# Kernel tuning notes

Hardware: AMD Instinct MI355X
Metric: run time of the kernel (lower is better)

The kernel has to match this reference:

```python
import jax, jax.numpy as jnp
import numpy as np

PATCH_SIZE = 24
ALPHA = 0.2  # LeakyReLU negative slope


def setup_inputs() -> dict:
    key = jax.random.key(0)
    k_x, k_adj, k_w, k_wc = jax.random.split(key, 4)
    B, T, N, Cin, Cout = 2, 96, 64, 16, 32
    x = jax.random.normal(k_x, (B, T, N, Cin), dtype=jnp.float32)
    adj = jax.random.uniform(k_adj, (N, N), dtype=jnp.float32)  # weighted adjacency in [0,1)
    # xavier_uniform with gain=1.414 on (Cin, Cout)
    limit = 1.414 * float(np.sqrt(6.0 / (Cin + Cout)))
    W = jax.random.uniform(k_w, (Cin, Cout), dtype=jnp.float32, minval=-limit, maxval=limit)
    W_c = jax.random.uniform(k_wc, (Cout,), dtype=jnp.float32, minval=-0.1, maxval=0.1)
    return {"x": x, "adj": adj, "W": W, "W_c": W_c}


def reference(x, adj, W, W_c):
    B, T, N, Cin = x.shape
    P = PATCH_SIZE
    NP = T // P
    Cout = W.shape[1]
    # torch.view semantics == row-major jnp.reshape (faithful, even though it mixes axes)
    x_patched = x.reshape(B, NP, N, P, Cin)
    h = x_patched @ W  # (B, NP, N, P, Cout)
    # vectorized over patches: per-patch outer product over nodes
    e = jnp.einsum('bsipc,bsjpc->bsijpc', h, h)  # (B, NP, N, N, P, Cout)
    e = jnp.where(e >= 0, e, ALPHA * e)  # LeakyReLU
    e = e * adj[None, None, :, :, None, None]
    e = jax.nn.softmax(e, axis=-1)  # softmax over channel dim (as in original)
    # torch.stack(list, dim=4) of (b,i,j,p,c) over patch index -> (B,N,N,P,NP,C)
    e = jnp.transpose(e, (0, 2, 3, 4, 1, 5))
    attention = e.reshape(B, N, N, T, Cout)  # (B, N, N, T, Cout)
    # h_patched.permute(0,2,1,3,4).reshape(B,N,T,C)
    h_flat = jnp.transpose(h, (0, 2, 1, 3, 4)).reshape(B, N, T, Cout)
    # einsum('bnqtc,bntc->bntc') == sum over q then elementwise multiply
    h_prime = attention.sum(axis=2) * h_flat
    return attention, jax.nn.elu(h_prime)
```

## Files before the change

kernel.cpp:

```cpp
#include <hip/hip_runtime.h>
#include <math.h>

#define Bq 2
#define Tq 96
#define Nq 64
#define CIN 16
#define COUT 32
#define PATCH 24
#define NPq 4
#define JC 4
#define JPER (Nq / JC)
#define ATT_SIZE (Bq * Nq * Nq * Tq * COUT)
#define HP_SIZE (Bq * Nq * Tq * COUT)
#define H_ROWS (Bq * NPq * Nq * PATCH)

__global__ __launch_bounds__(256) void h_gemm_kernel(
    const float* __restrict__ x, const float* __restrict__ W,
    float* __restrict__ h) {
    __shared__ float Wl[CIN * COUT];
    __shared__ float xs[8 * CIN];
    int tid = threadIdx.x;
    Wl[tid]       = W[tid];
    Wl[tid + 256] = W[tid + 256];
    if (tid < 8 * CIN) xs[tid] = x[blockIdx.x * (8 * CIN) + tid];
    __syncthreads();
    int rl = tid >> 5;
    int c  = tid & 31;
    float acc = 0.f;
#pragma unroll
    for (int k = 0; k < CIN; ++k)
        acc += xs[rl * CIN + k] * Wl[k * COUT + c];
    h[blockIdx.x * 256 + tid] = acc;
}

__global__ __launch_bounds__(384) void att_kernel(
    const float* __restrict__ h, const float* __restrict__ adj,
    float* __restrict__ att, float* __restrict__ part) {
    const int bi  = blockIdx.x;
    const int jc  = bi >> 9;
    const int r   = bi & 511;
    const int i   = r & 63;
    const int s   = (r >> 6) & 3;
    const int b   = r >> 8;
    const int j0  = jc * JPER;
    const int tid = threadIdx.x;
    const int p   = tid >> 4;
    const int c0  = (tid & 15) * 2;

    __shared__ float adjrow[JPER];
    if (tid < JPER) adjrow[tid] = adj[i * Nq + j0 + tid];
    __syncthreads();

    const float* hb = h + (size_t)((b * NPq + s) * Nq) * (PATCH * COUT);
    const float2 hi = *(const float2*)(hb + (i * PATCH + p) * COUT + c0);

    float acc0 = 0.f, acc1 = 0.f;
    size_t outbase = ((size_t)((b * Nq + i) * Nq + j0) * Tq + (p * NPq + s)) * COUT + c0;
    const size_t jstride = (size_t)Tq * COUT;

#pragma unroll 4
    for (int jj = 0; jj < JPER; ++jj) {
        const float2 hj = *(const float2*)(hb + ((j0 + jj) * PATCH + p) * COUT + c0);
        const float aj = adjrow[jj];

        float e0 = hi.x * hj.x;
        float e1 = hi.y * hj.y;
        e0 = fmaxf(e0, 0.2f * e0) * aj;
        e1 = fmaxf(e1, 0.2f * e1) * aj;

        float ex0 = __expf(e0);
        float ex1 = __expf(e1);
        float sm = ex0 + ex1;
#pragma unroll
        for (int d = 1; d < 16; d <<= 1) sm += __shfl_xor(sm, d);
        const float inv = __builtin_amdgcn_rcpf(sm);
        const float a0 = ex0 * inv;
        const float a1 = ex1 * inv;
        acc0 += a0;
        acc1 += a1;
        *(float2*)(att + outbase + (size_t)jj * jstride) = make_float2(a0, a1);
    }

    const int t = p * NPq + s;
    float* pp = part + (size_t)jc * HP_SIZE
                     + ((size_t)((b * Nq + i) * Tq + t)) * COUT + c0;
    *(float2*)pp = make_float2(acc0, acc1);
}

__global__ __launch_bounds__(256) void hprime_kernel(
    const float* __restrict__ part, const float* __restrict__ h,
    float* __restrict__ hprime) {
    const int vid  = blockIdx.x * 256 + threadIdx.x;
    const int base = vid * 4;
    const int c  = base & 31;
    const int t  = (base >> 5) % Tq;
    const int bi = base / (COUT * Tq);
    const int i  = bi & 63;
    const int b  = bi >> 6;

    float4 a0 = *(const float4*)(part + base);
    float4 a1 = *(const float4*)(part + base + HP_SIZE);
    float4 a2 = *(const float4*)(part + base + 2 * HP_SIZE);
    float4 a3 = *(const float4*)(part + base + 3 * HP_SIZE);

    const int s2 = t / PATCH;
    const int p2 = t % PATCH;
    const float4 hv = *(const float4*)(h + (size_t)((b * NPq + s2) * Nq + i) * (PATCH * COUT)
                                         + p2 * COUT + c);
    float v0 = (a0.x + a1.x + a2.x + a3.x) * hv.x;
    float v1 = (a0.y + a1.y + a2.y + a3.y) * hv.y;
    float v2 = (a0.z + a1.z + a2.z + a3.z) * hv.z;
    float v3 = (a0.w + a1.w + a2.w + a3.w) * hv.w;
    v0 = v0 >= 0.f ? v0 : expm1f(v0);
    v1 = v1 >= 0.f ? v1 : expm1f(v1);
    v2 = v2 >= 0.f ? v2 : expm1f(v2);
    v3 = v3 >= 0.f ? v3 : expm1f(v3);
    *(float4*)(hprime + base) = make_float4(v0, v1, v2, v3);
}

extern "C" void kernel_launch(void* const* d_in, const int* in_sizes, int n_in,
                              void* d_out, int out_size, void* d_ws, size_t ws_size,
                              hipStream_t stream) {
    (void)in_sizes; (void)n_in; (void)out_size; (void)ws_size;
    const float* x   = (const float*)d_in[0];
    const float* adj = (const float*)d_in[1];
    const float* W   = (const float*)d_in[2];

    float* h    = (float*)d_ws;
    float* part = (float*)d_ws + H_ROWS * COUT;
    float* att  = (float*)d_out;
    float* hp   = (float*)d_out + ATT_SIZE;

    hipLaunchKernelGGL(h_gemm_kernel, dim3(H_ROWS / 8), dim3(256), 0, stream,
                       x, W, h);
    hipLaunchKernelGGL(att_kernel, dim3(JC * Bq * NPq * Nq), dim3(384), 0, stream,
                       h, adj, att, part);
    hipLaunchKernelGGL(hprime_kernel, dim3(HP_SIZE / 4 / 256), dim3(256), 0, stream,
                       part, h, hp);
}
```

Measured before the change: 34.66 us.

## Fold patch index into block and widen attention stores to float4

The attention kernel now gives each thread 4 channels with float4 loads and stores, and moves the patch index s into the thread index, so each block covers all 4 patches. A warp's stores for one j now cover contiguous t rows (s then p), which gives fully contiguous 128B+ writes to the attention output. The softmax shuffle reduction drops from 4 to 3 steps. Blocks grow to 768 threads and the grid shrinks to 512 blocks, which may lower occupancy balance across CUs.

```diff
diff --git a/kernel.cpp b/kernel.cpp
--- a/kernel.cpp
+++ b/kernel.cpp
@@ -33,58 +33,58 @@
     h[blockIdx.x * 256 + tid] = acc;
 }
 
-__global__ __launch_bounds__(384) void att_kernel(
+__global__ __launch_bounds__(768) void att_kernel(
     const float* __restrict__ h, const float* __restrict__ adj,
     float* __restrict__ att, float* __restrict__ part) {
     const int bi  = blockIdx.x;
-    const int jc  = bi >> 9;
-    const int r   = bi & 511;
-    const int i   = r & 63;
-    const int s   = (r >> 6) & 3;
-    const int b   = r >> 8;
+    const int i   = bi & 63;
+    const int jc  = (bi >> 6) & 3;
+    const int b   = bi >> 8;
     const int j0  = jc * JPER;
     const int tid = threadIdx.x;
-    const int p   = tid >> 4;
-    const int c0  = (tid & 15) * 2;
+    const int c0  = (tid & 7) * 4;
+    const int s   = (tid >> 3) & 3;
+    const int p   = tid >> 5;
 
     __shared__ float adjrow[JPER];
     if (tid < JPER) adjrow[tid] = adj[i * Nq + j0 + tid];
     __syncthreads();
 
     const float* hb = h + (size_t)((b * NPq + s) * Nq) * (PATCH * COUT);
-    const float2 hi = *(const float2*)(hb + (i * PATCH + p) * COUT + c0);
+    const float4 hi = *(const float4*)(hb + (i * PATCH + p) * COUT + c0);
 
-    float acc0 = 0.f, acc1 = 0.f;
-    size_t outbase = ((size_t)((b * Nq + i) * Nq + j0) * Tq + (p * NPq + s)) * COUT + c0;
+    float4 acc = make_float4(0.f, 0.f, 0.f, 0.f);
+    const int t = p * NPq + s;
+    size_t outbase = ((size_t)((b * Nq + i) * Nq + j0) * Tq + t) * COUT + c0;
     const size_t jstride = (size_t)Tq * COUT;
 
 #pragma unroll 4
     for (int jj = 0; jj < JPER; ++jj) {
-        const float2 hj = *(const float2*)(hb + ((j0 + jj) * PATCH + p) * COUT + c0);
+        const float4 hj = *(const float4*)(hb + ((j0 + jj) * PATCH + p) * COUT + c0);
         const float aj = adjrow[jj];
 
-        float e0 = hi.x * hj.x;
-        float e1 = hi.y * hj.y;
+        float e0 = hi.x * hj.x, e1 = hi.y * hj.y;
+        float e2 = hi.z * hj.z, e3 = hi.w * hj.w;
         e0 = fmaxf(e0, 0.2f * e0) * aj;
         e1 = fmaxf(e1, 0.2f * e1) * aj;
+        e2 = fmaxf(e2, 0.2f * e2) * aj;
+        e3 = fmaxf(e3, 0.2f * e3) * aj;
 
-        float ex0 = __expf(e0);
-        float ex1 = __expf(e1);
-        float sm = ex0 + ex1;
+        const float x0 = __expf(e0), x1 = __expf(e1);
+        const float x2 = __expf(e2), x3 = __expf(e3);
+        float sm = (x0 + x1) + (x2 + x3);
 #pragma unroll
-        for (int d = 1; d < 16; d <<= 1) sm += __shfl_xor(sm, d);
+        for (int d = 1; d < 8; d <<= 1) sm += __shfl_xor(sm, d);
         const float inv = __builtin_amdgcn_rcpf(sm);
-        const float a0 = ex0 * inv;
-        const float a1 = ex1 * inv;
-        acc0 += a0;
-        acc1 += a1;
-        *(float2*)(att + outbase + (size_t)jj * jstride) = make_float2(a0, a1);
+        const float a0 = x0 * inv, a1 = x1 * inv;
+        const float a2 = x2 * inv, a3 = x3 * inv;
+        acc.x += a0; acc.y += a1; acc.z += a2; acc.w += a3;
+        *(float4*)(att + outbase + (size_t)jj * jstride) = make_float4(a0, a1, a2, a3);
     }
 
-    const int t = p * NPq + s;
     float* pp = part + (size_t)jc * HP_SIZE
                      + ((size_t)((b * Nq + i) * Tq + t)) * COUT + c0;
-    *(float2*)pp = make_float2(acc0, acc1);
+    *(float4*)pp = acc;
 }
 
 __global__ __launch_bounds__(256) void hprime_kernel(
@@ -133,7 +133,7 @@
 
     hipLaunchKernelGGL(h_gemm_kernel, dim3(H_ROWS / 8), dim3(256), 0, stream,
                        x, W, h);
-    hipLaunchKernelGGL(att_kernel, dim3(JC * Bq * NPq * Nq), dim3(384), 0, stream,
+    hipLaunchKernelGGL(att_kernel, dim3(Bq * JC * Nq), dim3(768), 0, stream,
                        h, adj, att, part);
     hipLaunchKernelGGL(hprime_kernel, dim3(HP_SIZE / 4 / 256), dim3(256), 0, stream,
                        part, h, hp);
```

Result: faster. 33.07 us (-4.6%).
